# Kernel optimization log

Measured on AMD Instinct MI355X. Metric: run time of the kernel, lower is better.

## Reference

```python
import jax, jax.numpy as jnp
import numpy as np
from jax.ops import segment_sum

N_NODES = 100000
N_EDGES = 1600000
HIDDEN = 64
N_LAYERS = 4
N_CLASSES = 10
N_GRAPHS = 512


def setup_inputs() -> dict:
    key = jax.random.key(0)
    ks = jax.random.split(key, 9)
    x = jax.random.normal(ks[0], (N_NODES, HIDDEN), dtype=jnp.float32)
    edge_index = jax.random.randint(ks[1], (2, N_EDGES), 0, N_NODES, dtype=jnp.int32)
    batch = jnp.sort(jax.random.randint(ks[2], (N_NODES,), 0, N_GRAPHS, dtype=jnp.int32))
    s = 0.05
    W_enc = jax.random.normal(ks[3], (HIDDEN, HIDDEN), dtype=jnp.float32) * s
    b_enc = jax.random.normal(ks[4], (HIDDEN,), dtype=jnp.float32) * s
    W_conv = jax.random.normal(ks[5], (N_LAYERS, HIDDEN, HIDDEN), dtype=jnp.float32) * s
    b_conv = jax.random.normal(ks[6], (N_LAYERS, HIDDEN), dtype=jnp.float32) * s
    W_out = jax.random.normal(ks[7], (HIDDEN, N_CLASSES), dtype=jnp.float32) * s
    b_out = jax.random.normal(ks[8], (N_CLASSES,), dtype=jnp.float32) * s
    return {"x": x, "edge_index": edge_index, "batch": batch,
            "W_enc": W_enc, "b_enc": b_enc, "W_conv": W_conv, "b_conv": b_conv,
            "W_out": W_out, "b_out": b_out, "num_graphs": N_GRAPHS}


def reference(x, edge_index, batch, W_enc, b_enc, W_conv, b_conv, W_out, b_out, num_graphs):
    N = x.shape[0]
    src, dst = edge_index[0], edge_index[1]
    # atom_encoder: Linear
    h = x @ W_enc + b_enc
    # GCN symmetric normalization with self-loops (PyG GCNConv default):
    # deg counts incoming edges (dst) plus the self-loop.
    deg = segment_sum(jnp.ones_like(src, dtype=h.dtype), dst, num_segments=N) + 1.0
    deg_inv_sqrt = jax.lax.rsqrt(deg)
    deg_inv = 1.0 / deg  # self-loop norm = d^-1/2 * d^-1/2
    edge_norm = (deg_inv_sqrt[src] * deg_inv_sqrt[dst])[:, None]  # [E,1]
    for l in range(W_conv.shape[0]):
        hl = h @ W_conv[l]                          # [N,H]
        msg = hl[src] * edge_norm                   # gather + normalize [E,H]
        agg = segment_sum(msg, dst, num_segments=N) # scatter-add
        h = agg + hl * deg_inv[:, None] + b_conv[l] # self-loop + bias
        h = jax.nn.silu(h)                          # dropout p=0 / eval: identity
    # global_add_pool over graph ids
    pooled = segment_sum(h, batch, num_segments=num_graphs)  # [G,H]
    # readout: Linear + ReLU (make_mlp with hidden_layers=1)
    out = jax.nn.relu(pooled @ W_out + b_out)
    return out
```

## Files before the change

kernel.cpp:

```cpp
#include <hip/hip_runtime.h>
#include <math.h>

#define HIDDEN 64
#define N_LAYERS 4
#define N_CLASSES 10
#define N_GRAPHS 512
#define BSH 8
#define NPB 256
#define PART_K 2048

typedef _Float16 __h;
typedef __attribute__((ext_vector_type(4))) _Float16 half4;
typedef __attribute__((ext_vector_type(8))) _Float16 half8;
typedef __attribute__((ext_vector_type(4))) float f32x4;

__global__ __launch_bounds__(256) void k_histA(const int* __restrict__ dst,
                                               int* __restrict__ ghist, int E, int NB) {
    __shared__ int hist[512];
    int t = threadIdx.x;
    hist[t] = 0; hist[t + 256] = 0;
    __syncthreads();
    int base = blockIdx.x * PART_K;
    int kend = min(PART_K, E - base);
    for (int k = t; k < kend; k += 256) atomicAdd(&hist[dst[base + k] >> BSH], 1);
    __syncthreads();
    for (int j = t; j < NB; j += 256) {
        int h = hist[j];
        if (h) atomicAdd(&ghist[j], h);
    }
}

__global__ __launch_bounds__(256) void k_bucketscan(const int* __restrict__ ghist,
                                                    int* __restrict__ bucketbase,
                                                    int* __restrict__ gcur, int NB) {
    __shared__ int s[256];
    int t = threadIdx.x;
    int j0 = 2 * t, j1 = 2 * t + 1;
    int h0 = (j0 < NB) ? ghist[j0] : 0;
    int h1 = (j1 < NB) ? ghist[j1] : 0;
    s[t] = h0 + h1; __syncthreads();
    for (int o = 1; o < 256; o <<= 1) {
        int x = (t >= o) ? s[t - o] : 0;
        __syncthreads();
        s[t] += x;
        __syncthreads();
    }
    int base = (t == 0) ? 0 : s[t - 1];
    if (j0 <= NB) { bucketbase[j0] = base;      gcur[j0] = base; }
    if (j1 <= NB) { bucketbase[j1] = base + h0; gcur[j1] = base + h0; }
}

__global__ __launch_bounds__(256) void k_partition(const int* __restrict__ src,
                                                   const int* __restrict__ dst,
                                                   int* __restrict__ gcur,
                                                   int* __restrict__ packed,
                                                   int E, int NB) {
    __shared__ int hist[512];
    __shared__ int scanE[512];
    __shared__ int cur[512];
    __shared__ int delta[512];
    __shared__ int ps[256];
    __shared__ int stage[PART_K];
    int t = threadIdx.x;
    int base = blockIdx.x * PART_K;
    int kend = min(PART_K, E - base);

    hist[t] = 0; hist[t + 256] = 0;
    __syncthreads();
    for (int k = t; k < kend; k += 256) atomicAdd(&hist[dst[base + k] >> BSH], 1);
    __syncthreads();

    int j0 = 2 * t, j1 = j0 + 1;
    int h0 = hist[j0], h1 = hist[j1];
    ps[t] = h0 + h1; __syncthreads();
    for (int o = 1; o < 256; o <<= 1) {
        int x = (t >= o) ? ps[t - o] : 0;
        __syncthreads();
        ps[t] += x;
        __syncthreads();
    }
    int bexc = (t == 0) ? 0 : ps[t - 1];
    scanE[j0] = bexc;
    scanE[j1] = bexc + h0;
    __syncthreads();

    for (int j = t; j < NB; j += 256) {
        int h = hist[j];
        int g = h ? atomicAdd(&gcur[j], h) : 0;
        delta[j] = g - scanE[j];
        cur[j]   = scanE[j];
    }
    __syncthreads();

    for (int k = t; k < kend; k += 256) {
        int d = dst[base + k], s = src[base + k];
        int j = d >> BSH;
        int pos = atomicAdd(&cur[j], 1);
        stage[pos] = (s << BSH) | (d & (NPB - 1));
    }
    __syncthreads();

    for (int i = t; i < kend; i += 256) {
        int lo = 0, hi = NB;
        while (hi - lo > 1) {
            int mid = (lo + hi) >> 1;
            if (scanE[mid] <= i) lo = mid; else hi = mid;
        }
        packed[i + delta[lo]] = stage[i];
    }
}

__global__ __launch_bounds__(256) void k_fill3(const int* __restrict__ packed,
                                               const int* __restrict__ bucketbase,
                                               int* __restrict__ rowptr,
                                               float* __restrict__ dis,
                                               int* __restrict__ csr_src,
                                               int N, int E) {
    __shared__ int cnt[256];
    __shared__ int rp[256];
    int j = blockIdx.x;
    int t = threadIdx.x;
    int node0 = j << BSH;
    int segb = bucketbase[j];
    int sege = bucketbase[j + 1];

    cnt[t] = 0; __syncthreads();
    for (int i = segb + t; i < sege; i += 256) atomicAdd(&cnt[packed[i] & (NPB - 1)], 1);
    __syncthreads();

    int c = cnt[t];
    rp[t] = c; __syncthreads();
    for (int o = 1; o < 256; o <<= 1) {
        int x = (t >= o) ? rp[t - o] : 0;
        __syncthreads();
        rp[t] += x;
        __syncthreads();
    }
    int node = node0 + t;
    int start = segb + rp[t] - c + node;
    if (node < N) {
        rowptr[node] = start;
        dis[node] = rsqrtf((float)c + 1.0f);
        csr_src[start] = node;
        if (node == N - 1) rowptr[N] = E + N;
    }
    __syncthreads();
    cnt[t] = start + 1;
    __syncthreads();
    for (int i = segb + t; i < sege; i += 256) {
        int v = packed[i];
        int slot = atomicAdd(&cnt[v & (NPB - 1)], 1);
        csr_src[slot] = v >> BSH;
    }
}

__device__ __forceinline__ half4 shfl_xor_h4(half4 v, int m) {
    uint2 u = __builtin_bit_cast(uint2, v);
    u.x = __shfl_xor((int)u.x, m);
    u.y = __shfl_xor((int)u.y, m);
    return __builtin_bit_cast(half4, u);
}

__global__ __launch_bounds__(256) void k_prepW(const float* __restrict__ Wconv,
                                               const float* __restrict__ Wenc,
                                               __h* __restrict__ Wh) {
    int idx = blockIdx.x * 256 + threadIdx.x;
    int l = idx >> 12;
    int kn = idx & 4095;
    int k = kn >> 6, n = kn & 63;
    int nt = n >> 4, nl = n & 15;
    int kt = k >> 5, kr = k & 31;
    int quad = kr >> 3, j = kr & 7;
    int lane = quad * 16 + nl;
    int pos = (((nt * 2 + kt) * 64 + lane) << 3) + j;
    float w = (l < N_LAYERS) ? Wconv[(size_t)l * 4096 + kn] : Wenc[kn];
    Wh[(l << 12) + pos] = (__h)w;
}

__global__ __launch_bounds__(256) void k_gather(const int* __restrict__ csr_src,
                                                const int* __restrict__ rowptr,
                                                const float* __restrict__ dis,
                                                const __h* __restrict__ G,
                                                __h* __restrict__ AGG, int N) {
    int node = blockIdx.x * 4 + (threadIdx.x >> 6);
    if (node >= N) return;
    int lane = threadIdx.x & 63;
    int grp  = lane >> 4;
    int f4   = lane & 15;
    int beg  = rowptr[node];
    int end  = rowptr[node + 1];

    const half4 z = {(__h)0.f, (__h)0.f, (__h)0.f, (__h)0.f};
    half4 a = z;
    int e = beg + grp;
    while (e < end) {
        int s0 = csr_src[e];
        int s1 = (e + 4  < end) ? csr_src[e + 4]  : -1;
        int s2 = (e + 8  < end) ? csr_src[e + 8]  : -1;
        int s3 = (e + 12 < end) ? csr_src[e + 12] : -1;
        int s4 = (e + 16 < end) ? csr_src[e + 16] : -1;
        int s5 = (e + 20 < end) ? csr_src[e + 20] : -1;
        int s6 = (e + 24 < end) ? csr_src[e + 24] : -1;
        int s7 = (e + 28 < end) ? csr_src[e + 28] : -1;
        half4 r0 = ((const half4*)(G + (size_t)s0 * 64))[f4];
        half4 r1 = (s1 >= 0) ? ((const half4*)(G + (size_t)s1 * 64))[f4] : z;
        half4 r2 = (s2 >= 0) ? ((const half4*)(G + (size_t)s2 * 64))[f4] : z;
        half4 r3 = (s3 >= 0) ? ((const half4*)(G + (size_t)s3 * 64))[f4] : z;
        half4 r4 = (s4 >= 0) ? ((const half4*)(G + (size_t)s4 * 64))[f4] : z;
        half4 r5 = (s5 >= 0) ? ((const half4*)(G + (size_t)s5 * 64))[f4] : z;
        half4 r6 = (s6 >= 0) ? ((const half4*)(G + (size_t)s6 * 64))[f4] : z;
        half4 r7 = (s7 >= 0) ? ((const half4*)(G + (size_t)s7 * 64))[f4] : z;
        a += r0; a += r1; a += r2; a += r3;
        a += r4; a += r5; a += r6; a += r7;
        e += 32;
    }
    a += shfl_xor_h4(a, 16);
    a += shfl_xor_h4(a, 32);

    if (grp == 0) {
        __h dd = (__h)dis[node];
        half4 o = a * dd;
        ((half4*)(AGG + (size_t)node * 64))[f4] = o;
    }
}

__global__ __launch_bounds__(256) void k_gemm_mfma(const __h* __restrict__ in,
                                                   const float* __restrict__ xf,
                                                   const __h* __restrict__ Wh,
                                                   const float* __restrict__ bias,
                                                   const float* __restrict__ dis,
                                                   const int* __restrict__ batch,
                                                   __h* __restrict__ Gho,
                                                   float* __restrict__ pooled,
                                                   int N, int mode) {
    int wave = threadIdx.x >> 6;
    int lane = threadIdx.x & 63;
    int row0 = (blockIdx.x * 4 + wave) * 32;
    if (row0 >= N) return;
    int quad = lane >> 4, nl = lane & 15;

    half8 bf[4][2];
    #pragma unroll
    for (int nt = 0; nt < 4; ++nt)
        #pragma unroll
        for (int kt = 0; kt < 2; ++kt)
            bf[nt][kt] = *(const half8*)(Wh + (((nt * 2 + kt) * 64 + lane) << 3));

    f32x4 acc[2][4];
    #pragma unroll
    for (int h = 0; h < 2; ++h) {
        int r = row0 + h * 16 + nl; if (r >= N) r = N - 1;
        half8 a0, a1;
        if (mode == 0) {
            const float* ap = xf + (size_t)r * 64 + quad * 8;
            float4 v0 = ((const float4*)ap)[0];
            float4 v1 = ((const float4*)ap)[1];
            float4 v2 = ((const float4*)(ap + 32))[0];
            float4 v3 = ((const float4*)(ap + 32))[1];
            a0 = (half8){(__h)v0.x, (__h)v0.y, (__h)v0.z, (__h)v0.w,
                         (__h)v1.x, (__h)v1.y, (__h)v1.z, (__h)v1.w};
            a1 = (half8){(__h)v2.x, (__h)v2.y, (__h)v2.z, (__h)v2.w,
                         (__h)v3.x, (__h)v3.y, (__h)v3.z, (__h)v3.w};
        } else {
            const __h* ap = in + (size_t)r * 64 + quad * 8;
            a0 = *(const half8*)(ap);
            a1 = *(const half8*)(ap + 32);
        }
        #pragma unroll
        for (int nt = 0; nt < 4; ++nt) {
            acc[h][nt] = (f32x4){0.f, 0.f, 0.f, 0.f};
            acc[h][nt] = __builtin_amdgcn_mfma_f32_16x16x32_f16(a0, bf[nt][0], acc[h][nt], 0, 0, 0);
            acc[h][nt] = __builtin_amdgcn_mfma_f32_16x16x32_f16(a1, bf[nt][1], acc[h][nt], 0, 0, 0);
        }
    }

    float b[4];
    #pragma unroll
    for (int nt = 0; nt < 4; ++nt) b[nt] = bias[nt * 16 + nl];

    if (mode != 2) {
        #pragma unroll
        for (int h = 0; h < 2; ++h) {
            #pragma unroll
            for (int reg = 0; reg < 4; ++reg) {
                int rr = row0 + h * 16 + quad * 4 + reg;
                if (rr < N) {
                    float ds = dis[rr];
                    #pragma unroll
                    for (int nt = 0; nt < 4; ++nt) {
                        float v = acc[h][nt][reg] + b[nt];
                        if (mode == 1) v = v / (1.0f + expf(-v));
                        Gho[(size_t)rr * 64 + nt * 16 + nl] = (__h)(ds * v);
                    }
                }
            }
        }
    } else {
        float run[4] = {0.f, 0.f, 0.f, 0.f};
        int cur = -1;
        #pragma unroll
        for (int h = 0; h < 2; ++h) {
            #pragma unroll
            for (int reg = 0; reg < 4; ++reg) {
                int rr = row0 + h * 16 + quad * 4 + reg;
                if (rr < N) {
                    int bi = batch[rr];
                    float vals[4];
                    #pragma unroll
                    for (int nt = 0; nt < 4; ++nt) {
                        float v = acc[h][nt][reg] + b[nt];
                        vals[nt] = v / (1.0f + expf(-v));
                    }
                    if (bi != cur) {
                        if (cur >= 0) {
                            #pragma unroll
                            for (int nt = 0; nt < 4; ++nt)
                                atomicAdd(&pooled[cur * 64 + nt * 16 + nl], run[nt]);
                        }
                        cur = bi;
                        #pragma unroll
                        for (int nt = 0; nt < 4; ++nt) run[nt] = vals[nt];
                    } else {
                        #pragma unroll
                        for (int nt = 0; nt < 4; ++nt) run[nt] += vals[nt];
                    }
                }
            }
        }
        if (cur >= 0) {
            #pragma unroll
            for (int nt = 0; nt < 4; ++nt)
                atomicAdd(&pooled[cur * 64 + nt * 16 + nl], run[nt]);
        }
    }
}

__global__ __launch_bounds__(256) void k_readout(const float* __restrict__ pooled,
                                                 const float* __restrict__ Wout,
                                                 const float* __restrict__ bout,
                                                 float* __restrict__ out) {
    int idx = blockIdx.x * 256 + threadIdx.x;
    if (idx >= N_GRAPHS * N_CLASSES) return;
    int g = idx / N_CLASSES, c = idx % N_CLASSES;
    float s = bout[c];
    #pragma unroll
    for (int j = 0; j < 64; ++j) s += pooled[g * 64 + j] * Wout[j * N_CLASSES + c];
    out[idx] = fmaxf(s, 0.0f);
}

extern "C" void kernel_launch(void* const* d_in, const int* in_sizes, int n_in,
                              void* d_out, int out_size, void* d_ws, size_t ws_size,
                              hipStream_t stream) {
    const float* x      = (const float*)d_in[0];
    const int*   ei     = (const int*)d_in[1];
    const int*   batch  = (const int*)d_in[2];
    const float* W_enc  = (const float*)d_in[3];
    const float* b_enc  = (const float*)d_in[4];
    const float* W_conv = (const float*)d_in[5];
    const float* b_conv = (const float*)d_in[6];
    const float* W_out  = (const float*)d_in[7];
    const float* b_out  = (const float*)d_in[8];
    float* out = (float*)d_out;

    const int N = in_sizes[2];
    const int E = in_sizes[1] / 2;
    const int* src = ei;
    const int* dst = ei + E;
    const int NB   = (N + NPB - 1) >> BSH;
    const int NBLK = (E + PART_K - 1) / PART_K;

    char* ws = (char*)d_ws;
    size_t off = 0;
    auto alloc = [&](size_t bytes) -> char* {
        char* p = ws + off;
        off += (bytes + 255) & ~(size_t)255;
        return p;
    };
    int*   ghist      = (int*)alloc((size_t)(NB + 1) * sizeof(int));
    int*   bucketbase = (int*)alloc((size_t)(NB + 1) * sizeof(int));
    int*   gcur       = (int*)alloc((size_t)(NB + 1) * sizeof(int));
    int*   packed     = (int*)alloc((size_t)E * sizeof(int));
    int*   csr_src    = (int*)alloc((size_t)(E + N) * sizeof(int));
    int*   rowptr     = (int*)alloc((size_t)(N + 1) * sizeof(int));
    float* dis        = (float*)alloc((size_t)N * sizeof(float));
    __h*   GhA        = (__h*)alloc((size_t)N * HIDDEN * sizeof(__h));
    __h*   AGGh       = (__h*)alloc((size_t)N * HIDDEN * sizeof(__h));
    __h*   Wh         = (__h*)alloc((size_t)(N_LAYERS + 1) * 4096 * sizeof(__h));
    float* pooled     = (float*)alloc((size_t)N_GRAPHS * HIDDEN * sizeof(float));
    (void)ws_size;

    hipMemsetAsync(ghist, 0, (size_t)(NB + 1) * sizeof(int), stream);
    hipMemsetAsync(pooled, 0, (size_t)N_GRAPHS * HIDDEN * sizeof(float), stream);

    k_histA     <<<NBLK, 256, 0, stream>>>(dst, ghist, E, NB);
    k_bucketscan<<<1,    256, 0, stream>>>(ghist, bucketbase, gcur, NB);
    k_partition <<<NBLK, 256, 0, stream>>>(src, dst, gcur, packed, E, NB);
    k_fill3     <<<NB,   256, 0, stream>>>(packed, bucketbase, rowptr, dis, csr_src, N, E);
    k_prepW<<<((N_LAYERS + 1) * 4096) / 256, 256, 0, stream>>>(W_conv, W_enc, Wh);

    int gb32 = (N + 127) / 128;
    k_gemm_mfma<<<gb32, 256, 0, stream>>>(nullptr, x, Wh + (size_t)N_LAYERS * 4096, b_enc,
                                          dis, batch, GhA, pooled, N, 0);

    for (int l = 0; l < N_LAYERS; ++l) {
        int last = (l == N_LAYERS - 1);
        k_gather<<<(N + 3) / 4, 256, 0, stream>>>(csr_src, rowptr, dis, GhA, AGGh, N);
        k_gemm_mfma<<<gb32, 256, 0, stream>>>(AGGh, nullptr, Wh + (size_t)l * 4096,
                                              b_conv + (size_t)l * HIDDEN, dis, batch,
                                              GhA, pooled, N, last ? 2 : 1);
    }

    k_readout<<<(N_GRAPHS * N_CLASSES + 255) / 256, 256, 0, stream>>>(pooled, W_out, b_out, out);
}
```

Before: 386.1 us.

## Fuse neighbor gather into MFMA layer GEMM with ping-pong feature buffers

Merges the per-layer gather and GEMM kernels into one kernel. Each lane gathers the half8 fragments of its own node's neighbors straight into MFMA A-operand registers, padding with a zeroed sentinel row at index N. This removes the AGG intermediate write and read and one launch per layer, and double buffers G to avoid read/write hazards. The cost is that each wave processes 16 nodes per half, looping to the maximum degree among them, which causes load imbalance, and there is less memory-level parallelism per node than the old 4-way split gather.

```diff
diff --git a/kernel.cpp b/kernel.cpp
--- a/kernel.cpp
+++ b/kernel.cpp
@@ -154,13 +154,6 @@
     }
 }
 
-__device__ __forceinline__ half4 shfl_xor_h4(half4 v, int m) {
-    uint2 u = __builtin_bit_cast(uint2, v);
-    u.x = __shfl_xor((int)u.x, m);
-    u.y = __shfl_xor((int)u.y, m);
-    return __builtin_bit_cast(half4, u);
-}
-
 __global__ __launch_bounds__(256) void k_prepW(const float* __restrict__ Wconv,
                                                const float* __restrict__ Wenc,
                                                __h* __restrict__ Wh) {
@@ -170,69 +163,18 @@
     int k = kn >> 6, n = kn & 63;
     int nt = n >> 4, nl = n & 15;
     int kt = k >> 5, kr = k & 31;
-    int quad = kr >> 3, j = kr & 7;
+    int quad = kr >> 3, jj = kr & 7;
     int lane = quad * 16 + nl;
-    int pos = (((nt * 2 + kt) * 64 + lane) << 3) + j;
+    int pos = (((nt * 2 + kt) * 64 + lane) << 3) + jj;
     float w = (l < N_LAYERS) ? Wconv[(size_t)l * 4096 + kn] : Wenc[kn];
     Wh[(l << 12) + pos] = (__h)w;
 }
 
-__global__ __launch_bounds__(256) void k_gather(const int* __restrict__ csr_src,
-                                                const int* __restrict__ rowptr,
-                                                const float* __restrict__ dis,
-                                                const __h* __restrict__ G,
-                                                __h* __restrict__ AGG, int N) {
-    int node = blockIdx.x * 4 + (threadIdx.x >> 6);
-    if (node >= N) return;
-    int lane = threadIdx.x & 63;
-    int grp  = lane >> 4;
-    int f4   = lane & 15;
-    int beg  = rowptr[node];
-    int end  = rowptr[node + 1];
-
-    const half4 z = {(__h)0.f, (__h)0.f, (__h)0.f, (__h)0.f};
-    half4 a = z;
-    int e = beg + grp;
-    while (e < end) {
-        int s0 = csr_src[e];
-        int s1 = (e + 4  < end) ? csr_src[e + 4]  : -1;
-        int s2 = (e + 8  < end) ? csr_src[e + 8]  : -1;
-        int s3 = (e + 12 < end) ? csr_src[e + 12] : -1;
-        int s4 = (e + 16 < end) ? csr_src[e + 16] : -1;
-        int s5 = (e + 20 < end) ? csr_src[e + 20] : -1;
-        int s6 = (e + 24 < end) ? csr_src[e + 24] : -1;
-        int s7 = (e + 28 < end) ? csr_src[e + 28] : -1;
-        half4 r0 = ((const half4*)(G + (size_t)s0 * 64))[f4];
-        half4 r1 = (s1 >= 0) ? ((const half4*)(G + (size_t)s1 * 64))[f4] : z;
-        half4 r2 = (s2 >= 0) ? ((const half4*)(G + (size_t)s2 * 64))[f4] : z;
-        half4 r3 = (s3 >= 0) ? ((const half4*)(G + (size_t)s3 * 64))[f4] : z;
-        half4 r4 = (s4 >= 0) ? ((const half4*)(G + (size_t)s4 * 64))[f4] : z;
-        half4 r5 = (s5 >= 0) ? ((const half4*)(G + (size_t)s5 * 64))[f4] : z;
-        half4 r6 = (s6 >= 0) ? ((const half4*)(G + (size_t)s6 * 64))[f4] : z;
-        half4 r7 = (s7 >= 0) ? ((const half4*)(G + (size_t)s7 * 64))[f4] : z;
-        a += r0; a += r1; a += r2; a += r3;
-        a += r4; a += r5; a += r6; a += r7;
-        e += 32;
-    }
-    a += shfl_xor_h4(a, 16);
-    a += shfl_xor_h4(a, 32);
-
-    if (grp == 0) {
-        __h dd = (__h)dis[node];
-        half4 o = a * dd;
-        ((half4*)(AGG + (size_t)node * 64))[f4] = o;
-    }
-}
-
-__global__ __launch_bounds__(256) void k_gemm_mfma(const __h* __restrict__ in,
-                                                   const float* __restrict__ xf,
-                                                   const __h* __restrict__ Wh,
-                                                   const float* __restrict__ bias,
-                                                   const float* __restrict__ dis,
-                                                   const int* __restrict__ batch,
-                                                   __h* __restrict__ Gho,
-                                                   float* __restrict__ pooled,
-                                                   int N, int mode) {
+__global__ __launch_bounds__(256) void k_enc(const float* __restrict__ xf,
+                                             const __h* __restrict__ Wh,
+                                             const float* __restrict__ bias,
+                                             const float* __restrict__ dis,
+                                             __h* __restrict__ Gho, int N) {
     int wave = threadIdx.x >> 6;
     int lane = threadIdx.x & 63;
     int row0 = (blockIdx.x * 4 + wave) * 32;
@@ -250,22 +192,15 @@
     #pragma unroll
     for (int h = 0; h < 2; ++h) {
         int r = row0 + h * 16 + nl; if (r >= N) r = N - 1;
-        half8 a0, a1;
-        if (mode == 0) {
-            const float* ap = xf + (size_t)r * 64 + quad * 8;
-            float4 v0 = ((const float4*)ap)[0];
-            float4 v1 = ((const float4*)ap)[1];
-            float4 v2 = ((const float4*)(ap + 32))[0];
-            float4 v3 = ((const float4*)(ap + 32))[1];
-            a0 = (half8){(__h)v0.x, (__h)v0.y, (__h)v0.z, (__h)v0.w,
-                         (__h)v1.x, (__h)v1.y, (__h)v1.z, (__h)v1.w};
-            a1 = (half8){(__h)v2.x, (__h)v2.y, (__h)v2.z, (__h)v2.w,
-                         (__h)v3.x, (__h)v3.y, (__h)v3.z, (__h)v3.w};
-        } else {
-            const __h* ap = in + (size_t)r * 64 + quad * 8;
-            a0 = *(const half8*)(ap);
-            a1 = *(const half8*)(ap + 32);
-        }
+        const float* ap = xf + (size_t)r * 64 + quad * 8;
+        float4 v0 = ((const float4*)ap)[0];
+        float4 v1 = ((const float4*)ap)[1];
+        float4 v2 = ((const float4*)(ap + 32))[0];
+        float4 v3 = ((const float4*)(ap + 32))[1];
+        half8 a0 = (half8){(__h)v0.x, (__h)v0.y, (__h)v0.z, (__h)v0.w,
+                           (__h)v1.x, (__h)v1.y, (__h)v1.z, (__h)v1.w};
+        half8 a1 = (half8){(__h)v2.x, (__h)v2.y, (__h)v2.z, (__h)v2.w,
+                           (__h)v3.x, (__h)v3.y, (__h)v3.z, (__h)v3.w};
         #pragma unroll
         for (int nt = 0; nt < 4; ++nt) {
             acc[h][nt] = (f32x4){0.f, 0.f, 0.f, 0.f};
@@ -277,10 +212,92 @@
     float b[4];
     #pragma unroll
     for (int nt = 0; nt < 4; ++nt) b[nt] = bias[nt * 16 + nl];
-
-    if (mode != 2) {
-        #pragma unroll
-        for (int h = 0; h < 2; ++h) {
+    #pragma unroll
+    for (int h = 0; h < 2; ++h)
+        #pragma unroll
+        for (int reg = 0; reg < 4; ++reg) {
+            int rr = row0 + h * 16 + quad * 4 + reg;
+            if (rr < N) {
+                float ds = dis[rr];
+                #pragma unroll
+                for (int nt = 0; nt < 4; ++nt)
+                    Gho[(size_t)rr * 64 + nt * 16 + nl] = (__h)(ds * (acc[h][nt][reg] + b[nt]));
+            }
+        }
+}
+
+__global__ __launch_bounds__(256) void k_layer(const int* __restrict__ csr_src,
+                                               const int* __restrict__ rowptr,
+                                               const float* __restrict__ dis,
+                                               const __h* __restrict__ G,
+                                               const __h* __restrict__ Wh,
+                                               const float* __restrict__ bias,
+                                               const int* __restrict__ batch,
+                                               __h* __restrict__ Gout,
+                                               float* __restrict__ pooled,
+                                               int N, int last) {
+    int wave = threadIdx.x >> 6;
+    int lane = threadIdx.x & 63;
+    int row0 = (blockIdx.x * 4 + wave) * 32;
+    if (row0 >= N) return;
+    int quad = lane >> 4, nl = lane & 15;
+
+    half8 bf[4][2];
+    #pragma unroll
+    for (int nt = 0; nt < 4; ++nt)
+        #pragma unroll
+        for (int kt = 0; kt < 2; ++kt)
+            bf[nt][kt] = *(const half8*)(Wh + (((nt * 2 + kt) * 64 + lane) << 3));
+
+    f32x4 acc[2][4];
+    #pragma unroll
+    for (int h = 0; h < 2; ++h) {
+        int node = row0 + h * 16 + nl;
+        if (node >= N) node = N - 1;
+        int beg = rowptr[node];
+        int len = rowptr[node + 1] - beg;
+        int ml = len;
+        #pragma unroll
+        for (int m = 1; m < 16; m <<= 1) {
+            int o = __shfl_xor(ml, m);
+            ml = (o > ml) ? o : ml;
+        }
+
+        half8 sa = {(__h)0.f, (__h)0.f, (__h)0.f, (__h)0.f,
+                    (__h)0.f, (__h)0.f, (__h)0.f, (__h)0.f};
+        half8 sb = sa;
+        for (int j = 0; j < ml; j += 4) {
+            #pragma unroll
+            for (int u = 0; u < 4; ++u) {
+                int jj = j + u;
+                int cidx = beg + ((jj < len) ? jj : (len - 1));
+                int s = csr_src[cidx];
+                if (jj >= len) s = N;
+                const __h* gp = G + (size_t)s * 64 + quad * 8;
+                half8 r0 = *(const half8*)gp;
+                half8 r1 = *(const half8*)(gp + 32);
+                sa += r0;
+                sb += r1;
+            }
+        }
+        __h dd = (__h)dis[node];
+        half8 a0 = sa * dd;
+        half8 a1 = sb * dd;
+        #pragma unroll
+        for (int nt = 0; nt < 4; ++nt) {
+            acc[h][nt] = (f32x4){0.f, 0.f, 0.f, 0.f};
+            acc[h][nt] = __builtin_amdgcn_mfma_f32_16x16x32_f16(a0, bf[nt][0], acc[h][nt], 0, 0, 0);
+            acc[h][nt] = __builtin_amdgcn_mfma_f32_16x16x32_f16(a1, bf[nt][1], acc[h][nt], 0, 0, 0);
+        }
+    }
+
+    float b[4];
+    #pragma unroll
+    for (int nt = 0; nt < 4; ++nt) b[nt] = bias[nt * 16 + nl];
+
+    if (!last) {
+        #pragma unroll
+        for (int h = 0; h < 2; ++h)
             #pragma unroll
             for (int reg = 0; reg < 4; ++reg) {
                 int rr = row0 + h * 16 + quad * 4 + reg;
@@ -289,17 +306,16 @@
                     #pragma unroll
                     for (int nt = 0; nt < 4; ++nt) {
                         float v = acc[h][nt][reg] + b[nt];
-                        if (mode == 1) v = v / (1.0f + expf(-v));
-                        Gho[(size_t)rr * 64 + nt * 16 + nl] = (__h)(ds * v);
+                        v = v / (1.0f + expf(-v));
+                        Gout[(size_t)rr * 64 + nt * 16 + nl] = (__h)(ds * v);
                     }
                 }
             }
-        }
     } else {
         float run[4] = {0.f, 0.f, 0.f, 0.f};
         int cur = -1;
         #pragma unroll
-        for (int h = 0; h < 2; ++h) {
+        for (int h = 0; h < 2; ++h)
             #pragma unroll
             for (int reg = 0; reg < 4; ++reg) {
                 int rr = row0 + h * 16 + quad * 4 + reg;
@@ -326,7 +342,6 @@
                     }
                 }
             }
-        }
         if (cur >= 0) {
             #pragma unroll
             for (int nt = 0; nt < 4; ++nt)
@@ -383,14 +398,16 @@
     int*   csr_src    = (int*)alloc((size_t)(E + N) * sizeof(int));
     int*   rowptr     = (int*)alloc((size_t)(N + 1) * sizeof(int));
     float* dis        = (float*)alloc((size_t)N * sizeof(float));
-    __h*   GhA        = (__h*)alloc((size_t)N * HIDDEN * sizeof(__h));
-    __h*   AGGh       = (__h*)alloc((size_t)N * HIDDEN * sizeof(__h));
+    __h*   GhA        = (__h*)alloc((size_t)(N + 1) * HIDDEN * sizeof(__h));
+    __h*   GhB        = (__h*)alloc((size_t)(N + 1) * HIDDEN * sizeof(__h));
     __h*   Wh         = (__h*)alloc((size_t)(N_LAYERS + 1) * 4096 * sizeof(__h));
     float* pooled     = (float*)alloc((size_t)N_GRAPHS * HIDDEN * sizeof(float));
     (void)ws_size;
 
     hipMemsetAsync(ghist, 0, (size_t)(NB + 1) * sizeof(int), stream);
     hipMemsetAsync(pooled, 0, (size_t)N_GRAPHS * HIDDEN * sizeof(float), stream);
+    hipMemsetAsync(GhA + (size_t)N * HIDDEN, 0, HIDDEN * sizeof(__h), stream);
+    hipMemsetAsync(GhB + (size_t)N * HIDDEN, 0, HIDDEN * sizeof(__h), stream);
 
     k_histA     <<<NBLK, 256, 0, stream>>>(dst, ghist, E, NB);
     k_bucketscan<<<1,    256, 0, stream>>>(ghist, bucketbase, gcur, NB);
@@ -399,15 +416,17 @@
     k_prepW<<<((N_LAYERS + 1) * 4096) / 256, 256, 0, stream>>>(W_conv, W_enc, Wh);
 
     int gb32 = (N + 127) / 128;
-    k_gemm_mfma<<<gb32, 256, 0, stream>>>(nullptr, x, Wh + (size_t)N_LAYERS * 4096, b_enc,
-                                          dis, batch, GhA, pooled, N, 0);
-
+    k_enc<<<gb32, 256, 0, stream>>>(x, Wh + (size_t)N_LAYERS * 4096, b_enc, dis, GhA, N);
+
+    __h* gin = GhA;
+    __h* gout = GhB;
     for (int l = 0; l < N_LAYERS; ++l) {
         int last = (l == N_LAYERS - 1);
-        k_gather<<<(N + 3) / 4, 256, 0, stream>>>(csr_src, rowptr, dis, GhA, AGGh, N);
-        k_gemm_mfma<<<gb32, 256, 0, stream>>>(AGGh, nullptr, Wh + (size_t)l * 4096,
-                                              b_conv + (size_t)l * HIDDEN, dis, batch,
-                                              GhA, pooled, N, last ? 2 : 1);
+        k_layer<<<gb32, 256, 0, stream>>>(csr_src, rowptr, dis, gin,
+                                          Wh + (size_t)l * 4096,
+                                          b_conv + (size_t)l * HIDDEN, batch,
+                                          gout, pooled, N, last);
+        __h* t = gin; gin = gout; gout = t;
     }
 
     k_readout<<<(N_GRAPHS * N_CLASSES + 255) / 256, 256, 0, stream>>>(pooled, W_out, b_out, out);
```

After: 399.0 us. 1.03x slower.
